# Kernel optimization log

Hardware: AMD Instinct MI355X
Metric: run time of the kernel (lower is better)

The kernel has to match this reference:

```python
import jax, jax.numpy as jnp
import numpy as np

W_DIM = 512
LRELU_SLOPE = 0.2
ACT_GAIN = np.sqrt(2.0).astype(np.float32)  # def_gain for lrelu, gain=1


def setup_inputs() -> dict:
    key = jax.random.key(0)
    k1, k2, k3, k4 = jax.random.split(key, 4)
    B, Cin, Cout, R, K = 8, 128, 128, 32, 3
    return {
        "x": jax.random.normal(k1, (B, Cin, R, R, R), dtype=jnp.float32),
        "w": jax.random.normal(k2, (B, W_DIM), dtype=jnp.float32),
        "weight": jax.random.normal(k3, (Cout, Cin, K, K, K), dtype=jnp.float32),
        "affine_weight": jax.random.normal(k4, (Cin, W_DIM), dtype=jnp.float32),
        "affine_bias": jnp.ones((Cin,), dtype=jnp.float32),
        "bias": jnp.zeros((Cout,), dtype=jnp.float32),
    }


def _conv_one(xi, wi):
    # xi: [Cin, D, H, W], wi: [Cout, Cin, k, k, k] -> [Cout, D, H, W]
    return jax.lax.conv_general_dilated(
        xi[None], wi, window_strides=(1, 1, 1),
        padding=[(1, 1), (1, 1), (1, 1)],
        dimension_numbers=("NCDHW", "OIDHW", "NCDHW"))[0]


def reference(x, w, weight, affine_weight, affine_bias, bias):
    B = x.shape[0]
    # affine: FullyConnectedLayer, linear, weight_gain = 1/sqrt(w_dim), bias_gain=1
    styles = w @ (affine_weight * (1.0 / np.sqrt(W_DIM))).T + affine_bias  # [B, Cin]
    # modulate
    wmod = weight[None] * styles[:, None, :, None, None, None]  # [B, Cout, Cin, k, k, k]
    # demodulate
    dcoefs = jax.lax.rsqrt(jnp.sum(jnp.square(wmod), axis=(2, 3, 4, 5)) + 1e-8)  # [B, Cout]
    wmod = wmod * dcoefs[:, :, None, None, None, None]
    # grouped conv (groups = batch) == vmap of per-sample conv
    out = jax.vmap(_conv_one)(x, wmod)  # [B, Cout, R, R, R]
    # bias_act: lrelu with gain=sqrt(2), clamp=None (noise path is disabled in forward)
    out = out + bias[None, :, None, None, None]
    out = jnp.where(out >= 0, out, out * LRELU_SLOPE) * ACT_GAIN
    return out
```

## Files before the change

kernel.cpp:

```cpp
#include <hip/hip_runtime.h>
#include <hip/hip_bf16.h>

typedef __attribute__((ext_vector_type(8))) short bf16x8;
typedef __attribute__((ext_vector_type(4))) float f32x4;

#define WDIM 512
#define CIN 128
#define COUT 128
#define NRES 32
#define NSP 32768
#define NTAPS 27

#define ROWB 2112
#define LDSROWS 16
#define BUFB (LDSROWS * ROWB)

#define ZP_OFF 4096
#define XT_OFF 8192
#define WM_OFF (8192 + 67108864)

typedef __attribute__((address_space(1))) const unsigned int gu32;
typedef __attribute__((address_space(3))) unsigned int lu32;

__global__ __launch_bounds__(256)
void k_wmod(const float* __restrict__ w,
            const float* __restrict__ aw,
            const float* __restrict__ ab,
            const float* __restrict__ weight,
            float* __restrict__ zeropad,
            __hip_bfloat16* __restrict__ wmod) {
  int b = blockIdx.x >> 7;
  int co = blockIdx.x & 127;
  int tid = threadIdx.x;
  if (blockIdx.x == 0) {
#pragma unroll
    for (int i = 0; i < 4; i++) zeropad[i * 256 + tid] = 0.f;
  }
  __shared__ float stp[256];
  __shared__ float st[CIN];
  __shared__ float red[4];
  {
    int c = tid & 127, half = tid >> 7;
    const float4* wr = (const float4*)(w + (size_t)b * WDIM + half * 256);
    const float4* ar = (const float4*)(aw + (size_t)c * WDIM + half * 256);
    float s = 0.f;
#pragma unroll 8
    for (int k = 0; k < 64; k++) {
      float4 wv = wr[k], av = ar[k];
      s += wv.x * av.x + wv.y * av.y + wv.z * av.z + wv.w * av.w;
    }
    stp[tid] = s;
  }
  __syncthreads();
  if (tid < 128)
    st[tid] = (stp[tid] + stp[tid + 128]) * 0.04419417382415922f + ab[tid];
  __syncthreads();
  const float* wr = weight + (size_t)co * (CIN * NTAPS);
  float ss = 0.f;
  for (int o = tid; o < CIN * NTAPS; o += 256) {
    float v = wr[o] * st[o / NTAPS];
    ss += v * v;
  }
#pragma unroll
  for (int off = 32; off > 0; off >>= 1) ss += __shfl_down(ss, off);
  if ((tid & 63) == 0) red[tid >> 6] = ss;
  __syncthreads();
  float d = rsqrtf(red[0] + red[1] + red[2] + red[3] + 1e-8f);
  for (int o = tid; o < CIN * NTAPS; o += 256) {
    int t = o >> 7;
    int cin = o & 127;
    float v = wr[cin * NTAPS + t] * st[cin] * d;
    int cc = cin >> 5, cl = cin & 31;
    wmod[((((size_t)(b * 4 + cc) * COUT + co) * NTAPS + t) << 5) + cl] =
        __float2bfloat16(v);
  }
}

__global__ __launch_bounds__(256)
void k_xt(const float* __restrict__ x, __hip_bfloat16* __restrict__ xt) {
  __shared__ __align__(16) float ts[32][257];
  int t = threadIdx.x;
  int blk = blockIdx.x;
  int b = blk >> 9, cc = (blk >> 7) & 3, sp0 = (blk & 127) << 8;
  const float* xb = x + (size_t)b * CIN * NSP + (size_t)cc * 32 * NSP + sp0;
#pragma unroll
  for (int i = 0; i < 8; i++) {
    int q = i * 256 + t;
    int cin = q >> 6, f4 = q & 63;
    float4 v = *(const float4*)(xb + (size_t)cin * NSP + f4 * 4);
    *(float4*)&ts[cin][f4 * 4] = v;
  }
  __syncthreads();
  __hip_bfloat16* ob = xt + ((size_t)(b * 4 + cc) * NSP + sp0) * 32;
#pragma unroll
  for (int j = 0; j < 4; j++) {
    int chunk = j * 256 + t;
    int sp_l = chunk >> 2, q = chunk & 3;
    union { bf16x8 v; __hip_bfloat16 h[8]; } u;
#pragma unroll
    for (int k = 0; k < 8; k++) u.h[k] = __float2bfloat16(ts[q * 8 + k][sp_l]);
    *(bf16x8*)(ob + (size_t)sp_l * 32 + q * 8) = u.v;
  }
}

__global__ __launch_bounds__(256, 2)
void k_conv(const char* __restrict__ ws,
            const float* __restrict__ bias,
            float* __restrict__ out) {
  extern __shared__ __align__(16) char xs[];

  int tid = threadIdx.x;
  int lane = tid & 63, w = tid >> 6;
  int l15 = lane & 15, g = lane >> 4;
  int blk = blockIdx.x;
  int b = blk & 7;
  int tile = blk >> 3;
  int z0 = (tile >> 4) * 2, y0 = (tile & 15) * 2;

  {
    int r16 = tid >> 4, c16 = (tid & 15) * 4;
    *(int*)&xs[r16 * ROWB + 2048 + c16] = 0;
    *(int*)&xs[BUFB + r16 * ROWB + 2048 + c16] = 0;
  }

  int soff[8], sdst[8], svalid[8];
#pragma unroll
  for (int i = 0; i < 8; i++) {
    int c = i * 256 + tid;
    int zy = c >> 7;
    int hz = zy >> 2, hy = zy & 3;
    int zz = z0 + hz - 1, yy = y0 + hy - 1;
    svalid[i] = ((unsigned)zz < NRES) & ((unsigned)yy < NRES);
    int p = c & 127, hx = p >> 2, pos = p & 3;
    int q = pos ^ ((hx >> 1) & 3);
    soff[i] = (zz * 1024 + yy * 32 + hx) * 4 + q;
    sdst[i] = zy * ROWB + (p >> 6) * 1024;
  }

  int vaddr[8][3];
#pragma unroll
  for (int ni = 0; ni < 8; ni++) {
    int row = (ni >> 2) * 4 + ((ni >> 1) & 1);
    int dx = (ni & 1) * 16 + l15;
#pragma unroll
    for (int tx = 0; tx < 3; tx++) {
      int hx = dx + tx - 1;
      int hxc = ((unsigned)hx > 31u) ? 32 : hx;
      int pos = g ^ ((hxc >> 1) & 3);
      vaddr[ni][tx] = row * ROWB + hxc * 64 + pos * 16;
    }
  }

  const bf16x8* ap = (const bf16x8*)(ws + WM_OFF);
  int abase[2];
#pragma unroll
  for (int mi = 0; mi < 2; mi++)
    abase[mi] = (w * 32 + mi * 16 + l15) * 108 + g;

  f32x4 acc[2][8];
#pragma unroll
  for (int mi = 0; mi < 2; mi++)
#pragma unroll
    for (int ni = 0; ni < 8; ni++) acc[mi][ni] = (f32x4){0.f, 0.f, 0.f, 0.f};

  const char* zpg = ws + ZP_OFF;
  const char* xtb = ws + XT_OFF + (size_t)b * (4 * NSP * 64);

  auto stage = [&](char* dst, const char* xtc) {
#pragma unroll
    for (int i = 0; i < 8; i++) {
      const char* src = svalid[i] ? (xtc + ((size_t)(unsigned)soff[i] << 4))
                                  : (zpg + lane * 16);
      __builtin_amdgcn_global_load_lds((gu32*)src, (lu32*)(dst + sdst[i]), 16, 0, 0);
    }
  };

  stage(xs, xtb);
  __syncthreads();

#pragma unroll 1
  for (int cc = 0; cc < 4; cc++) {
    char* cur = xs + (cc & 1) * BUFB;
    int sab = ((b * 4 + cc) * 128) * 108;
    int abc0 = sab + abase[0], abc1 = sab + abase[1];

    bf16x8 A[4][2], B[2][8];
#pragma unroll
    for (int pt = 0; pt < 4; pt++) {
      A[pt][0] = ap[abc0 + pt * 4];
      A[pt][1] = ap[abc1 + pt * 4];
    }
#pragma unroll
    for (int j = 0; j < 8; j++) B[0][j] = *(const bf16x8*)(cur + vaddr[j][0]);
    __builtin_amdgcn_sched_barrier(0);
    if (cc < 3)
      stage(xs + ((cc + 1) & 1) * BUFB, xtb + (size_t)(cc + 1) * (NSP * 64));
    __builtin_amdgcn_sched_barrier(0);

#pragma unroll
    for (int t = 0; t < NTAPS; t++) {
      const int s = t & 3;
      const int sb = t & 1, nsb = sb ^ 1;
      if (t < NTAPS - 1) {
        const int t1 = t + 1;
        const int tx1 = t1 % 3;
        const int lit1 = ((t1 / 9) * 4 + (t1 / 3) % 3) * ROWB;
#pragma unroll
        for (int j = 0; j < 8; j++)
          B[nsb][j] = *(const bf16x8*)(cur + vaddr[j][tx1] + lit1);
      }
      __builtin_amdgcn_s_setprio(1);
#pragma unroll
      for (int mi = 0; mi < 2; mi++) {
        acc[mi][0] = __builtin_amdgcn_mfma_f32_16x16x32_bf16(A[s][mi], B[sb][0], acc[mi][0], 0, 0, 0);
        acc[mi][1] = __builtin_amdgcn_mfma_f32_16x16x32_bf16(A[s][mi], B[sb][1], acc[mi][1], 0, 0, 0);
        acc[mi][2] = __builtin_amdgcn_mfma_f32_16x16x32_bf16(A[s][mi], B[sb][2], acc[mi][2], 0, 0, 0);
        acc[mi][3] = __builtin_amdgcn_mfma_f32_16x16x32_bf16(A[s][mi], B[sb][3], acc[mi][3], 0, 0, 0);
        acc[mi][4] = __builtin_amdgcn_mfma_f32_16x16x32_bf16(A[s][mi], B[sb][4], acc[mi][4], 0, 0, 0);
        acc[mi][5] = __builtin_amdgcn_mfma_f32_16x16x32_bf16(A[s][mi], B[sb][5], acc[mi][5], 0, 0, 0);
        acc[mi][6] = __builtin_amdgcn_mfma_f32_16x16x32_bf16(A[s][mi], B[sb][6], acc[mi][6], 0, 0, 0);
        acc[mi][7] = __builtin_amdgcn_mfma_f32_16x16x32_bf16(A[s][mi], B[sb][7], acc[mi][7], 0, 0, 0);
      }
      __builtin_amdgcn_s_setprio(0);
      if (t + 4 < NTAPS) {
        A[s][0] = ap[abc0 + (t + 4) * 4];
        A[s][1] = ap[abc1 + (t + 4) * 4];
      }
    }
    if (cc < 3) __syncthreads();
  }

  size_t ob = ((size_t)(b * COUT + w * 32 + g * 4)) * NSP +
              (size_t)z0 * 1024 + (size_t)y0 * 32;
#pragma unroll
  for (int mi = 0; mi < 2; mi++) {
    float4 bsv = *(const float4*)(bias + w * 32 + mi * 16 + g * 4);
    float bs[4] = {bsv.x, bsv.y, bsv.z, bsv.w};
#pragma unroll
    for (int ni = 0; ni < 8; ni++) {
      int spo = (ni >> 2) * 1024 + ((ni >> 1) & 1) * 32 + (ni & 1) * 16 + l15;
#pragma unroll
      for (int r = 0; r < 4; r++) {
        float v = acc[mi][ni][r] + bs[r];
        v = (v >= 0.f ? v : v * 0.2f) * 1.41421356237309515f;
        out[ob + (size_t)(mi * 16 + r) * NSP + spo] = v;
      }
    }
  }
}

extern "C" void kernel_launch(void* const* d_in, const int* in_sizes, int n_in,
                              void* d_out, int out_size, void* d_ws, size_t ws_size,
                              hipStream_t stream) {
  const float* x      = (const float*)d_in[0];
  const float* w      = (const float*)d_in[1];
  const float* weight = (const float*)d_in[2];
  const float* aw     = (const float*)d_in[3];
  const float* ab     = (const float*)d_in[4];
  const float* bias   = (const float*)d_in[5];
  float* out = (float*)d_out;

  float* zeropad = (float*)((char*)d_ws + ZP_OFF);
  __hip_bfloat16* xt = (__hip_bfloat16*)((char*)d_ws + XT_OFF);
  __hip_bfloat16* wmod = (__hip_bfloat16*)((char*)d_ws + WM_OFF);

  k_wmod<<<8 * 128, 256, 0, stream>>>(w, aw, ab, weight, zeropad, wmod);
  k_xt<<<8 * 4 * 128, 256, 0, stream>>>(x, xt);
  k_conv<<<8 * 256, 256, 2 * BUFB, stream>>>((const char*)d_ws, bias, out);
}
```

Before: 260.0 us.

## Deepen LDS B-fragment prefetch to two taps and rotate channel-chunk order per block

The conv main loop now keeps three B register buffers and prefetches LDS fragments two taps ahead instead of one, so LDS latency has more time to hide behind MFMAs. Half of the blocks also start at channel chunk 2 instead of 0, which spreads global and L2 traffic across different input-channel slabs. This adds 8 bf16x8 registers per thread, which could cause spills or lower occupancy under the 2-blocks launch bound.

```diff
diff --git a/kernel.cpp b/kernel.cpp
--- a/kernel.cpp
+++ b/kernel.cpp
@@ -116,6 +116,7 @@
   int b = blk & 7;
   int tile = blk >> 3;
   int z0 = (tile >> 4) * 2, y0 = (tile & 15) * 2;
+  int ccrot = ((blk >> 8) & 1) * 2;
 
   {
     int r16 = tid >> 4, c16 = (tid & 15) * 4;
@@ -175,39 +176,46 @@
     }
   };
 
-  stage(xs, xtb);
+  stage(xs, xtb + (size_t)ccrot * (NSP * 64));
   __syncthreads();
 
 #pragma unroll 1
-  for (int cc = 0; cc < 4; cc++) {
-    char* cur = xs + (cc & 1) * BUFB;
+  for (int cc0 = 0; cc0 < 4; cc0++) {
+    const int cc = (cc0 + ccrot) & 3;
+    char* cur = xs + (cc0 & 1) * BUFB;
     int sab = ((b * 4 + cc) * 128) * 108;
     int abc0 = sab + abase[0], abc1 = sab + abase[1];
 
-    bf16x8 A[4][2], B[2][8];
+    bf16x8 A[4][2], B[3][8];
 #pragma unroll
     for (int pt = 0; pt < 4; pt++) {
       A[pt][0] = ap[abc0 + pt * 4];
       A[pt][1] = ap[abc1 + pt * 4];
     }
 #pragma unroll
-    for (int j = 0; j < 8; j++) B[0][j] = *(const bf16x8*)(cur + vaddr[j][0]);
+    for (int pt = 0; pt < 2; pt++) {
+#pragma unroll
+      for (int j = 0; j < 8; j++)
+        B[pt][j] = *(const bf16x8*)(cur + vaddr[j][pt]);
+    }
     __builtin_amdgcn_sched_barrier(0);
-    if (cc < 3)
-      stage(xs + ((cc + 1) & 1) * BUFB, xtb + (size_t)(cc + 1) * (NSP * 64));
+    if (cc0 < 3) {
+      const int ccn = (cc0 + 1 + ccrot) & 3;
+      stage(xs + ((cc0 + 1) & 1) * BUFB, xtb + (size_t)ccn * (NSP * 64));
+    }
     __builtin_amdgcn_sched_barrier(0);
 
 #pragma unroll
     for (int t = 0; t < NTAPS; t++) {
       const int s = t & 3;
-      const int sb = t & 1, nsb = sb ^ 1;
-      if (t < NTAPS - 1) {
-        const int t1 = t + 1;
-        const int tx1 = t1 % 3;
-        const int lit1 = ((t1 / 9) * 4 + (t1 / 3) % 3) * ROWB;
+      const int sb = t % 3;
+      if (t + 2 < NTAPS) {
+        const int t2 = t + 2;
+        const int tx2 = t2 % 3;
+        const int lit2 = ((t2 / 9) * 4 + (t2 / 3) % 3) * ROWB;
 #pragma unroll
         for (int j = 0; j < 8; j++)
-          B[nsb][j] = *(const bf16x8*)(cur + vaddr[j][tx1] + lit1);
+          B[t2 % 3][j] = *(const bf16x8*)(cur + vaddr[j][tx2] + lit2);
       }
       __builtin_amdgcn_s_setprio(1);
 #pragma unroll
@@ -227,7 +235,7 @@
         A[s][1] = ap[abc1 + (t + 4) * 4];
       }
     }
-    if (cc < 3) __syncthreads();
+    if (cc0 < 3) __syncthreads();
   }
 
   size_t ob = ((size_t)(b * COUT + w * 32 + g * 4)) * NSP +
```

Result: no change. 259.4 us (-0.2%).
